# Kernel optimization log

Hardware: AMD Instinct MI355X
Metric: run time of the kernel (lower is better)

## Reference

```python
import jax, jax.numpy as jnp
import numpy as np

D_MODEL = 768
NUM_HEADS = 12
D_K = D_MODEL // NUM_HEADS  # 64


def setup_inputs() -> dict:
    key = jax.random.key(0)
    ks = jax.random.split(key, 7)
    B, S = 2, 4096
    Q = jax.random.normal(ks[0], (B, S, D_MODEL), dtype=jnp.float32)
    K = jax.random.normal(ks[1], (B, S, D_MODEL), dtype=jnp.float32)
    V = jax.random.normal(ks[2], (B, S, D_MODEL), dtype=jnp.float32)
    scale = 1.0 / np.sqrt(D_MODEL)
    # Per-head projection weights stacked: [H, d_model, d_k] (equivalent to
    # the torch per-head nn.Linear(d_model, d_k, bias=False) applied as x @ W)
    WQ = jax.random.normal(ks[3], (NUM_HEADS, D_MODEL, D_K), dtype=jnp.float32) * scale
    WK = jax.random.normal(ks[4], (NUM_HEADS, D_MODEL, D_K), dtype=jnp.float32) * scale
    WV = jax.random.normal(ks[5], (NUM_HEADS, D_MODEL, D_K), dtype=jnp.float32) * scale
    # Output projection: [num_head*d_v, d_model]
    WO = jax.random.normal(ks[6], (NUM_HEADS * D_K, D_MODEL), dtype=jnp.float32) * scale
    return {"Q": Q, "K": K, "V": V, "WQ": WQ, "WK": WK, "WV": WV, "WO": WO}


def reference(Q, K, V, WQ, WK, WV, WO):
    # Per-head projections (batched over heads): [B,H,S,d_k]
    q = jnp.einsum('bsd,hdk->bhsk', Q, WQ)
    k = jnp.einsum('bsd,hdk->bhsk', K, WK)
    v = jnp.einsum('bsd,hdk->bhsk', V, WV)
    # Full attention scores: [B,H,S,S]
    scores = jnp.einsum('bhqd,bhsd->bhqs', q, k) / jnp.sqrt(jnp.asarray(D_K, q.dtype))
    attn = jax.nn.softmax(scores, axis=-1)  # dropout_p=0 -> identity
    out = jnp.einsum('bhqs,bhsd->bhqd', attn, v)  # [B,H,S,d_k]
    # Concatenate heads along feature dim (head order = concat order)
    B, H, S, Dk = out.shape
    out = out.transpose(0, 2, 1, 3).reshape(B, S, H * Dk)
    return out @ WO  # [B,S,d_model]
```

## Files before the change

### kernel.cpp

```cpp
#include <hip/hip_runtime.h>
#include <hip/hip_bf16.h>
#include <stdint.h>
#include <stddef.h>

#define NH 12
#define DKH 64
#define DM 768
#define SS 4096

typedef __attribute__((ext_vector_type(8))) short bf16x8;
typedef __attribute__((ext_vector_type(4))) float f32x4;
typedef __attribute__((ext_vector_type(16))) float f32x16;

__device__ __forceinline__ unsigned short f2bf(float x) {
  union { float f; unsigned int u; } a; a.f = x;
  unsigned int r = a.u + 0x7fffu + ((a.u >> 16) & 1u);
  return (unsigned short)(r >> 16);
}

__device__ __forceinline__ unsigned pkbf2(float a, float b) {
  union { __hip_bfloat162 h; unsigned u; } x;
  x.h = __float22bfloat162_rn(float2{a, b});
  return x.u;
}

__device__ __forceinline__ unsigned cvt_pk_bf16(float lo, float hi) {
  unsigned r;
  asm("v_cvt_pk_bf16_f32 %0, %1, %2" : "=v"(r) : "v"(lo), "v"(hi));
  return r;
}

__device__ __forceinline__ void plane32_swap(unsigned& a, unsigned& b) {
  asm("v_permlane32_swap_b32 %0, %1" : "+v"(a), "+v"(b));
}

__device__ __forceinline__ float fast_exp2(float x) {
#if __has_builtin(__builtin_amdgcn_exp2f)
  return __builtin_amdgcn_exp2f(x);
#else
  return exp2f(x);
#endif
}

__device__ __forceinline__ unsigned comb2(unsigned pa, unsigned pb, float inv) {
  union { unsigned v; float f; } lo0, hi0, lo1, hi1;
  lo0.v = (pa & 0xffffu) << 16; hi0.v = pa & 0xffff0000u;
  lo1.v = (pb & 0xffffu) << 16; hi1.v = pb & 0xffff0000u;
  return pkbf2((lo0.f + lo1.f) * inv, (hi0.f + hi1.f) * inv);
}

__device__ __forceinline__ void gload16(const void* g, void* l) {
  __builtin_amdgcn_global_load_lds(
      (const __attribute__((address_space(1))) void*)g,
      (__attribute__((address_space(3))) void*)l, 16, 0, 0);
}

__global__ __launch_bounds__(256) void prep(
    const float* __restrict__ Q, const float* __restrict__ K,
    const float* __restrict__ V, const float* __restrict__ WQ,
    const float* __restrict__ WK, const float* __restrict__ WV,
    const float* __restrict__ WO, unsigned short* __restrict__ qkv,
    unsigned short* __restrict__ wq, unsigned short* __restrict__ wk,
    unsigned short* __restrict__ wv, unsigned short* __restrict__ wo) {
  int bx = blockIdx.x;
  if (bx < 9216) {
    int gid = bx * 256 + threadIdx.x;
    int t = gid / 786432, e = gid % 786432;
    const float* src = (t == 0) ? Q : (t == 1) ? K : V;
    float4 a = *(const float4*)(src + (size_t)e * 8);
    float4 c = *(const float4*)(src + (size_t)e * 8 + 4);
    union { unsigned u[4]; uint4 v; } o;
    o.u[0] = pkbf2(a.x, a.y); o.u[1] = pkbf2(a.z, a.w);
    o.u[2] = pkbf2(c.x, c.y); o.u[3] = pkbf2(c.z, c.w);
    *(uint4*)(qkv + (size_t)t * 6291456 + (size_t)e * 8) = o.v;
  } else {
    int idx = (bx - 9216) * 256 + threadIdx.x;
    if (idx >= DM * DM) return;
    int n = idx / DM, k = idx % DM;
    int src = ((n >> 6) * DM + k) * DKH + (n & 63);
    wq[idx] = f2bf(WQ[src] * 0.18033688011112042f);
    wk[idx] = f2bf(WK[src]);
    wv[idx] = f2bf(WV[src]);
    wo[idx] = f2bf(WO[k * DM + n]);
  }
}

__global__ __launch_bounds__(256, 2) void proj_gemm3(
    const unsigned short* __restrict__ Abase,
    const unsigned short* __restrict__ Wbase,
    unsigned short* __restrict__ Obase) {
  __shared__ unsigned short As[2][128 * 64];
  __shared__ unsigned short Bs[2][96 * 64];
  const int tid = threadIdx.x;
  const int lane = tid & 63, wave = tid >> 6;
  const int wm = wave >> 1, wn = wave & 1;
  const int l15 = lane & 15, lhi = lane >> 4;
  const int lrow = lane >> 3;
  const int schunk = (lane & 7) ^ lrow;

  int fid = blockIdx.x + (blockIdx.y << 3) + (blockIdx.z << 9);
  int nid = (fid & 7) * 192 + (fid >> 3);
  const int bx = nid & 7;
  const int rem = nid >> 3;
  const int by = rem & 63, z = rem >> 6;
  const bool z2 = (z == 2);

  const unsigned short* A = Abase + (size_t)z * 6291456;
  const unsigned short* Wt = Wbase + (size_t)z * DM * DM;
  unsigned short* out = Obase + (size_t)z * 2 * NH * SS * DKH;
  const int m0 = by * 128, n0 = bx * 96;

  auto stage = [&](int k0, int buf) {
#pragma unroll
    for (int i = 0; i < 4; ++i) {
      int r = wave * 32 + i * 8;
      gload16(A + (size_t)(m0 + r + lrow) * DM + k0 + schunk * 8, &As[buf][r * 64]);
    }
#pragma unroll
    for (int i = 0; i < 3; ++i) {
      int r = wave * 24 + i * 8;
      gload16(Wt + (size_t)(n0 + r + lrow) * DM + k0 + schunk * 8, &Bs[buf][r * 64]);
    }
  };

  f32x4 acc[4][3] = {};

  stage(0, 0);
  stage(64, 1);

  for (int t = 0; t < 12; ++t) {
    if (t < 11) asm volatile("s_waitcnt vmcnt(7)" ::: "memory");
    else        asm volatile("s_waitcnt vmcnt(0)" ::: "memory");
    asm volatile("s_barrier" ::: "memory");
    const int buf = t & 1;
    bf16x8 af[4][2], bfr[3][2];
#pragma unroll
    for (int m = 0; m < 4; ++m) {
      int row = wm * 64 + m * 16 + l15;
#pragma unroll
      for (int ks = 0; ks < 2; ++ks)
        af[m][ks] = *(const bf16x8*)&As[buf][row * 64 + (((ks * 4 + lhi) ^ (row & 7)) * 8)];
    }
#pragma unroll
    for (int n = 0; n < 3; ++n) {
      int row = wn * 48 + n * 16 + l15;
#pragma unroll
      for (int ks = 0; ks < 2; ++ks)
        bfr[n][ks] = *(const bf16x8*)&Bs[buf][row * 64 + (((ks * 4 + lhi) ^ (row & 7)) * 8)];
    }
    asm volatile("s_waitcnt lgkmcnt(0)" ::: "memory");
    asm volatile("s_barrier" ::: "memory");
    if (t + 2 < 12) stage((t + 2) * 64, buf);
    __builtin_amdgcn_s_setprio(1);
#pragma unroll
    for (int ks = 0; ks < 2; ++ks)
#pragma unroll
      for (int m = 0; m < 4; ++m)
#pragma unroll
        for (int n = 0; n < 3; ++n) {
          if (z2)
            acc[m][n] = __builtin_amdgcn_mfma_f32_16x16x32_bf16(bfr[n][ks], af[m][ks], acc[m][n], 0, 0, 0);
          else
            acc[m][n] = __builtin_amdgcn_mfma_f32_16x16x32_bf16(af[m][ks], bfr[n][ks], acc[m][n], 0, 0, 0);
        }
    __builtin_amdgcn_s_setprio(0);
  }

  if (!z2) {
#pragma unroll
    for (int m = 0; m < 4; ++m) {
#pragma unroll
      for (int r = 0; r < 4; ++r) {
        int row = m0 + wm * 64 + m * 16 + lhi * 4 + r;
        int bb = row >> 12, s = row & 4095;
#pragma unroll
        for (int n = 0; n < 3; ++n) {
          int col = n0 + wn * 48 + n * 16 + l15;
          int hh = col >> 6, dk = col & 63;
          out[((size_t)(bb * NH + hh) * SS + s) * DKH + dk] = f2bf(acc[m][n][r]);
        }
      }
    }
  } else {
#pragma unroll
    for (int m = 0; m < 4; ++m) {
      int srow = m0 + wm * 64 + m * 16 + l15;
      int bb = srow >> 12, s = srow & 4095;
#pragma unroll
      for (int n = 0; n < 3; ++n) {
#pragma unroll
        for (int r = 0; r < 4; ++r) {
          int col = n0 + wn * 48 + n * 16 + lhi * 4 + r;
          int hh = col >> 6, dk = col & 63;
          out[((size_t)(bb * NH + hh) * DKH + dk) * SS + s] = f2bf(acc[m][n][r]);
        }
      }
    }
  }
}

__device__ __forceinline__ void pack_pb(const f32x16& s0, const f32x16& s1, bf16x8* pb) {
#pragma unroll
  for (int h2 = 0; h2 < 2; ++h2) {
    unsigned c0a = cvt_pk_bf16(s0[8 * h2 + 0], s0[8 * h2 + 1]);
    unsigned c1a = cvt_pk_bf16(s0[8 * h2 + 2], s0[8 * h2 + 3]);
    unsigned c0b = cvt_pk_bf16(s0[8 * h2 + 4], s0[8 * h2 + 5]);
    unsigned c1b = cvt_pk_bf16(s0[8 * h2 + 6], s0[8 * h2 + 7]);
    plane32_swap(c0a, c0b);
    plane32_swap(c1a, c1b);
    union { unsigned u[4]; bf16x8 v; } f;
    f.u[0] = c0a; f.u[1] = c1a; f.u[2] = c0b; f.u[3] = c1b;
    pb[h2] = f.v;
  }
#pragma unroll
  for (int h2 = 0; h2 < 2; ++h2) {
    unsigned c0a = cvt_pk_bf16(s1[8 * h2 + 0], s1[8 * h2 + 1]);
    unsigned c1a = cvt_pk_bf16(s1[8 * h2 + 2], s1[8 * h2 + 3]);
    unsigned c0b = cvt_pk_bf16(s1[8 * h2 + 4], s1[8 * h2 + 5]);
    unsigned c1b = cvt_pk_bf16(s1[8 * h2 + 6], s1[8 * h2 + 7]);
    plane32_swap(c0a, c0b);
    plane32_swap(c1a, c1b);
    union { unsigned u[4]; bf16x8 v; } f;
    f.u[0] = c0a; f.u[1] = c1a; f.u[2] = c0b; f.u[3] = c1b;
    pb[2 + h2] = f.v;
  }
}

__device__ __forceinline__ float tree16(const f32x16& v) {
  float a = (v[0] + v[1]) + (v[2] + v[3]);
  float b = (v[4] + v[5]) + (v[6] + v[7]);
  float c = (v[8] + v[9]) + (v[10] + v[11]);
  float d = (v[12] + v[13]) + (v[14] + v[15]);
  return (a + b) + (c + d);
}

__global__ __launch_bounds__(256, 4) void flash_attn(
    const unsigned short* __restrict__ Qp, const unsigned short* __restrict__ Kp,
    const unsigned short* __restrict__ Vt, unsigned short* __restrict__ Opart,
    float* __restrict__ Lpart) {
  __shared__ unsigned short KV[2][8192];
  const int tid = threadIdx.x;
  const int lane = tid & 63, wave = tid >> 6;
  const int ql = lane & 31, hi = lane >> 5;

  int fid = blockIdx.x + (blockIdx.y << 5) + (blockIdx.z << 9) + (blockIdx.z << 8);
  int nid = (fid & 7) * 192 + (fid >> 3);
  const int qb = nid & 31;
  const int rem = nid >> 5;
  const int bh = rem % 24, split = rem / 24;
  const int q0w = qb * 128 + wave * 32;
  const int kvbase = split * (SS / 2);

  bf16x8 qf[4];
  {
    const unsigned short* qp = Qp + ((size_t)bh * SS + q0w + ql) * DKH;
#pragma unroll
    for (int s = 0; s < 4; ++s)
      qf[s] = *(const bf16x8*)(qp + s * 16 + hi * 8);
  }

  const unsigned short* gK = Kp + (size_t)bh * SS * DKH;
  const unsigned short* gV = Vt + (size_t)bh * DKH * SS;
  const int lrow = lane >> 3;
  const int sch = ((lane & 7) ^ lrow) * 8;
  const int xs = (ql & 7) << 3;

  auto stage = [&](int kv0, int buf) {
#pragma unroll
    for (int i = 0; i < 2; ++i) {
      int r = wave * 16 + i * 8;
      gload16(gK + (size_t)(kv0 + r + lrow) * DKH + sch, &KV[buf][r * 64]);
      gload16(gV + (size_t)(r + lrow) * SS + kv0 + sch, &KV[buf][4096 + r * 64]);
    }
  };

  stage(kvbase, 0);

  f32x16 oA = {}, oB = {};
  float lp = 0.f;
  const f32x16 zc = {};

  for (int it = 0; it < 32; ++it) {
    asm volatile("s_waitcnt vmcnt(0)" ::: "memory");
    __builtin_amdgcn_s_barrier();
    __builtin_amdgcn_sched_barrier(0);
    const int buf = it & 1;
    if (it + 1 < 32) stage(kvbase + (it + 1) * 64, buf ^ 1);
    const unsigned short* Ks = &KV[buf][0];
    const unsigned short* Vs = &KV[buf][4096];

    f32x16 s0, s1;
    __builtin_amdgcn_s_setprio(1);
    {
      bf16x8 ka0 = *(const bf16x8*)&Ks[ql * 64 + ((hi * 8) ^ xs)];
      bf16x8 ka1 = *(const bf16x8*)&Ks[(32 + ql) * 64 + ((hi * 8) ^ xs)];
      s0 = __builtin_amdgcn_mfma_f32_32x32x16_bf16(ka0, qf[0], zc, 0, 0, 0);
      s1 = __builtin_amdgcn_mfma_f32_32x32x16_bf16(ka1, qf[0], zc, 0, 0, 0);
    }
#pragma unroll
    for (int s = 1; s < 4; ++s) {
      bf16x8 ka0 = *(const bf16x8*)&Ks[ql * 64 + ((s * 16 + hi * 8) ^ xs)];
      bf16x8 ka1 = *(const bf16x8*)&Ks[(32 + ql) * 64 + ((s * 16 + hi * 8) ^ xs)];
      s0 = __builtin_amdgcn_mfma_f32_32x32x16_bf16(ka0, qf[s], s0, 0, 0, 0);
      s1 = __builtin_amdgcn_mfma_f32_32x32x16_bf16(ka1, qf[s], s1, 0, 0, 0);
    }
    __builtin_amdgcn_s_setprio(0);

#pragma unroll
    for (int r = 0; r < 16; ++r) s0[r] = fast_exp2(s0[r]);
#pragma unroll
    for (int r = 0; r < 16; ++r) s1[r] = fast_exp2(s1[r]);
    lp += tree16(s0) + tree16(s1);

    bf16x8 pb[4];
    pack_pb(s0, s1, pb);

    __builtin_amdgcn_s_setprio(1);
#pragma unroll
    for (int ks = 0; ks < 4; ++ks) {
      bf16x8 va0 = *(const bf16x8*)&Vs[ql * 64 + ((ks * 16 + hi * 8) ^ xs)];
      bf16x8 va1 = *(const bf16x8*)&Vs[(32 + ql) * 64 + ((ks * 16 + hi * 8) ^ xs)];
      oA = __builtin_amdgcn_mfma_f32_32x32x16_bf16(va0, pb[ks], oA, 0, 0, 0);
      oB = __builtin_amdgcn_mfma_f32_32x32x16_bf16(va1, pb[ks], oB, 0, 0, 0);
    }
    __builtin_amdgcn_s_setprio(0);
  }

  float l = lp + __shfl_xor(lp, 32);
  unsigned short* orow = Opart + ((size_t)(split * 24 + bh) * SS + q0w + ql) * DKH;
#pragma unroll
  for (int g = 0; g < 4; ++g) {
    int d0 = g * 8 + hi * 4;
    *(unsigned*)&orow[d0]          = cvt_pk_bf16(oA[4 * g + 0], oA[4 * g + 1]);
    *(unsigned*)&orow[d0 + 2]      = cvt_pk_bf16(oA[4 * g + 2], oA[4 * g + 3]);
    *(unsigned*)&orow[32 + d0]     = cvt_pk_bf16(oB[4 * g + 0], oB[4 * g + 1]);
    *(unsigned*)&orow[32 + d0 + 2] = cvt_pk_bf16(oB[4 * g + 2], oB[4 * g + 3]);
  }
  if (hi == 0) Lpart[(size_t)(split * 24 + bh) * SS + q0w + ql] = l;
}

__global__ __launch_bounds__(256, 2) void out_gemm(
    const unsigned short* __restrict__ Opart, const float* __restrict__ Lpart,
    const unsigned short* __restrict__ Wt, float* __restrict__ out) {
  __shared__ unsigned short As[2][64 * 64];
  __shared__ unsigned short Bs[2][128 * 64];
  const int tid = threadIdx.x;
  const int lane = tid & 63, wave = tid >> 6;
  const int wm = wave >> 1, wn = wave & 1;
  const int l15 = lane & 15, lhi = lane >> 4;
  const int lrow = lane >> 3;
  const int schunk = (lane & 7) ^ lrow;

  int fid = blockIdx.x + 6 * blockIdx.y;
  int nid = (fid & 7) * 96 + (fid >> 3);
  const int bx = nid % 6, by = nid / 6;
  const int m0 = by * 64, n0 = bx * 128;
  const int bB = m0 >> 12, s0 = m0 & 4095;

  const int arow = tid >> 2;
  const int acn = (tid & 3) * 2;
  const int aw0 = arow * 64 + ((acn ^ (arow & 7)) * 8);
  const int aw1 = arow * 64 + (((acn + 1) ^ (arow & 7)) * 8);
  const size_t PS = (size_t)24 * SS * DKH;
  const size_t LS = (size_t)24 * SS;

  auto stageAB = [&](int k0, int buf) {
    const int h = k0 >> 6;
    const size_t pbase = ((size_t)(bB * NH + h) * SS + s0 + arow) * 64 + acn * 8;
    uint4 a0 = *(const uint4*)(Opart + pbase);
    uint4 a1 = *(const uint4*)(Opart + pbase + 8);
    uint4 b0 = *(const uint4*)(Opart + PS + pbase);
    uint4 b1 = *(const uint4*)(Opart + PS + pbase + 8);
    const size_t lidx = (size_t)(bB * NH + h) * SS + s0 + arow;
    float la = Lpart[lidx], lb = Lpart[LS + lidx];
#pragma unroll
    for (int i = 0; i < 4; ++i) {
      int r = wave * 32 + i * 8;
      gload16(Wt + (size_t)(n0 + r + lrow) * DM + k0 + schunk * 8, &Bs[buf][r * 64]);
    }
    float inv = 1.0f / (la + lb);
    union { unsigned u[4]; uint4 v; } o0, o1;
    const unsigned* pa = (const unsigned*)&a0;
    const unsigned* pc = (const unsigned*)&b0;
#pragma unroll
    for (int i = 0; i < 4; ++i) o0.u[i] = comb2(pa[i], pc[i], inv);
    pa = (const unsigned*)&a1;
    pc = (const unsigned*)&b1;
#pragma unroll
    for (int i = 0; i < 4; ++i) o1.u[i] = comb2(pa[i], pc[i], inv);
    *(uint4*)&As[buf][aw0] = o0.v;
    *(uint4*)&As[buf][aw1] = o1.v;
  };

  f32x4 acc[2][4] = {};
  stageAB(0, 0);
  stageAB(64, 1);

  for (int t = 0; t < 12; ++t) {
    if (t < 11) asm volatile("s_waitcnt vmcnt(4) lgkmcnt(0)" ::: "memory");
    else        asm volatile("s_waitcnt vmcnt(0) lgkmcnt(0)" ::: "memory");
    asm volatile("s_barrier" ::: "memory");
    const int buf = t & 1;
    bf16x8 af[2][2], bfr[4][2];
#pragma unroll
    for (int m = 0; m < 2; ++m) {
      int row = wm * 32 + m * 16 + l15;
#pragma unroll
      for (int ks = 0; ks < 2; ++ks)
        af[m][ks] = *(const bf16x8*)&As[buf][row * 64 + (((ks * 4 + lhi) ^ (row & 7)) * 8)];
    }
#pragma unroll
    for (int n = 0; n < 4; ++n) {
      int row = wn * 64 + n * 16 + l15;
#pragma unroll
      for (int ks = 0; ks < 2; ++ks)
        bfr[n][ks] = *(const bf16x8*)&Bs[buf][row * 64 + (((ks * 4 + lhi) ^ (row & 7)) * 8)];
    }
    asm volatile("s_waitcnt lgkmcnt(0)" ::: "memory");
    asm volatile("s_barrier" ::: "memory");
    if (t + 2 < 12) stageAB((t + 2) * 64, buf);
    __builtin_amdgcn_s_setprio(1);
#pragma unroll
    for (int ks = 0; ks < 2; ++ks)
#pragma unroll
      for (int m = 0; m < 2; ++m)
#pragma unroll
        for (int n = 0; n < 4; ++n)
          acc[m][n] = __builtin_amdgcn_mfma_f32_16x16x32_bf16(af[m][ks], bfr[n][ks], acc[m][n], 0, 0, 0);
    __builtin_amdgcn_s_setprio(0);
  }

#pragma unroll
  for (int m = 0; m < 2; ++m)
#pragma unroll
    for (int r = 0; r < 4; ++r) {
      int row = m0 + wm * 32 + m * 16 + lhi * 4 + r;
#pragma unroll
      for (int n = 0; n < 4; ++n) {
        int col = n0 + wn * 64 + n * 16 + l15;
        out[(size_t)row * DM + col] = acc[m][n][r];
      }
    }
}

extern "C" void kernel_launch(void* const* d_in, const int* in_sizes, int n_in,
                              void* d_out, int out_size, void* d_ws, size_t ws_size,
                              hipStream_t stream) {
  const float* Q  = (const float*)d_in[0];
  const float* K  = (const float*)d_in[1];
  const float* V  = (const float*)d_in[2];
  const float* WQ = (const float*)d_in[3];
  const float* WK = (const float*)d_in[4];
  const float* WV = (const float*)d_in[5];
  const float* WO = (const float*)d_in[6];
  char* ws = (char*)d_ws;

  const size_t WSZ = (size_t)DM * DM * 2;
  const size_t ABF = (size_t)2 * SS * DM * 2;
  unsigned short* w_base  = (unsigned short*)(ws);
  unsigned short* wo_t    = (unsigned short*)(ws + 3 * WSZ);
  unsigned short* qkv_bf  = (unsigned short*)(ws + 4 * WSZ);
  unsigned short* p_base  = (unsigned short*)(ws + 4 * WSZ + 3 * ABF);
  unsigned short* q_p  = p_base;
  unsigned short* k_p  = p_base + ABF / 2;
  unsigned short* v_t  = p_base + ABF;
  unsigned short* opart = qkv_bf;
  float* lpart = (float*)(ws + 4 * WSZ + 2 * ABF);

  prep<<<9216 + 2304, 256, 0, stream>>>(
      Q, K, V, WQ, WK, WV, WO, qkv_bf,
      w_base, w_base + WSZ / 2, w_base + WSZ, wo_t);

  proj_gemm3<<<dim3(8, 64, 3), 256, 0, stream>>>(qkv_bf, w_base, p_base);

  flash_attn<<<dim3(32, 24, 2), 256, 0, stream>>>(q_p, k_p, v_t, opart, lpart);

  out_gemm<<<dim3(6, 128), 256, 0, stream>>>(opart, lpart, wo_t, (float*)d_out);
}
```

Before: 213.5 us.

## Defer partial-combine LDS writes past MFMAs and vectorize projection epilogue stores

```diff
diff --git a/kernel.cpp b/kernel.cpp
--- a/kernel.cpp
+++ b/kernel.cpp
@@ -157,28 +157,24 @@
 #pragma unroll
       for (int m = 0; m < 4; ++m)
 #pragma unroll
-        for (int n = 0; n < 3; ++n) {
-          if (z2)
-            acc[m][n] = __builtin_amdgcn_mfma_f32_16x16x32_bf16(bfr[n][ks], af[m][ks], acc[m][n], 0, 0, 0);
-          else
-            acc[m][n] = __builtin_amdgcn_mfma_f32_16x16x32_bf16(af[m][ks], bfr[n][ks], acc[m][n], 0, 0, 0);
-        }
+        for (int n = 0; n < 3; ++n)
+          acc[m][n] = __builtin_amdgcn_mfma_f32_16x16x32_bf16(bfr[n][ks], af[m][ks], acc[m][n], 0, 0, 0);
     __builtin_amdgcn_s_setprio(0);
   }
 
   if (!z2) {
 #pragma unroll
     for (int m = 0; m < 4; ++m) {
-#pragma unroll
-      for (int r = 0; r < 4; ++r) {
-        int row = m0 + wm * 64 + m * 16 + lhi * 4 + r;
-        int bb = row >> 12, s = row & 4095;
-#pragma unroll
-        for (int n = 0; n < 3; ++n) {
-          int col = n0 + wn * 48 + n * 16 + l15;
-          int hh = col >> 6, dk = col & 63;
-          out[((size_t)(bb * NH + hh) * SS + s) * DKH + dk] = f2bf(acc[m][n][r]);
-        }
+      int srow = m0 + wm * 64 + m * 16 + l15;
+      int bb = srow >> 12, s = srow & 4095;
+#pragma unroll
+      for (int n = 0; n < 3; ++n) {
+        int colb = n0 + wn * 48 + n * 16 + lhi * 4;
+        int hh = colb >> 6, dk = colb & 63;
+        union { unsigned short u[4]; uint2 v; } p;
+#pragma unroll
+        for (int r = 0; r < 4; ++r) p.u[r] = f2bf(acc[m][n][r]);
+        *(uint2*)&out[((size_t)(bb * NH + hh) * SS + s) * DKH + dk] = p.v;
       }
     }
   } else {
@@ -364,28 +360,36 @@
   const size_t PS = (size_t)24 * SS * DKH;
   const size_t LS = (size_t)24 * SS;
 
-  auto stageAB = [&](int k0, int buf) {
+  uint4 a0_, a1_, c0_, c1_;
+  float la_, lb_;
+
+  auto issueA = [&](int k0) {
     const int h = k0 >> 6;
     const size_t pbase = ((size_t)(bB * NH + h) * SS + s0 + arow) * 64 + acn * 8;
-    uint4 a0 = *(const uint4*)(Opart + pbase);
-    uint4 a1 = *(const uint4*)(Opart + pbase + 8);
-    uint4 b0 = *(const uint4*)(Opart + PS + pbase);
-    uint4 b1 = *(const uint4*)(Opart + PS + pbase + 8);
+    a0_ = *(const uint4*)(Opart + pbase);
+    a1_ = *(const uint4*)(Opart + pbase + 8);
+    c0_ = *(const uint4*)(Opart + PS + pbase);
+    c1_ = *(const uint4*)(Opart + PS + pbase + 8);
     const size_t lidx = (size_t)(bB * NH + h) * SS + s0 + arow;
-    float la = Lpart[lidx], lb = Lpart[LS + lidx];
+    la_ = Lpart[lidx];
+    lb_ = Lpart[LS + lidx];
+  };
+  auto issueB = [&](int k0, int buf) {
 #pragma unroll
     for (int i = 0; i < 4; ++i) {
       int r = wave * 32 + i * 8;
       gload16(Wt + (size_t)(n0 + r + lrow) * DM + k0 + schunk * 8, &Bs[buf][r * 64]);
     }
-    float inv = 1.0f / (la + lb);
+  };
+  auto commitA = [&](int buf) {
+    float inv = 1.0f / (la_ + lb_);
     union { unsigned u[4]; uint4 v; } o0, o1;
-    const unsigned* pa = (const unsigned*)&a0;
-    const unsigned* pc = (const unsigned*)&b0;
+    const unsigned* pa = (const unsigned*)&a0_;
+    const unsigned* pc = (const unsigned*)&c0_;
 #pragma unroll
     for (int i = 0; i < 4; ++i) o0.u[i] = comb2(pa[i], pc[i], inv);
-    pa = (const unsigned*)&a1;
-    pc = (const unsigned*)&b1;
+    pa = (const unsigned*)&a1_;
+    pc = (const unsigned*)&c1_;
 #pragma unroll
     for (int i = 0; i < 4; ++i) o1.u[i] = comb2(pa[i], pc[i], inv);
     *(uint4*)&As[buf][aw0] = o0.v;
@@ -393,8 +397,8 @@
   };
 
   f32x4 acc[2][4] = {};
-  stageAB(0, 0);
-  stageAB(64, 1);
+  issueA(0); issueB(0, 0); commitA(0);
+  issueA(64); issueB(64, 1); commitA(1);
 
   for (int t = 0; t < 12; ++t) {
     if (t < 11) asm volatile("s_waitcnt vmcnt(4) lgkmcnt(0)" ::: "memory");
@@ -418,7 +422,8 @@
     }
     asm volatile("s_waitcnt lgkmcnt(0)" ::: "memory");
     asm volatile("s_barrier" ::: "memory");
-    if (t + 2 < 12) stageAB((t + 2) * 64, buf);
+    const bool more = (t + 2 < 12);
+    if (more) { issueA((t + 2) * 64); issueB((t + 2) * 64, buf); }
     __builtin_amdgcn_s_setprio(1);
 #pragma unroll
     for (int ks = 0; ks < 2; ++ks)
@@ -428,6 +433,7 @@
         for (int n = 0; n < 4; ++n)
           acc[m][n] = __builtin_amdgcn_mfma_f32_16x16x32_bf16(af[m][ks], bfr[n][ks], acc[m][n], 0, 0, 0);
     __builtin_amdgcn_s_setprio(0);
+    if (more) commitA(buf);
   }
 
 #pragma unroll
```

Result: faster. 205.1 us (median of 2 runs) (-3.9%).
